# Kernel tuning notes

Measured on AMD Instinct MI355X. Metric: run time of the kernel, lower is better.

The kernel has to match this reference:

```python
import jax, jax.numpy as jnp
import numpy as np

N_HEADS = 16
D_MODEL = 1024
D_K = D_MODEL // N_HEADS
NEG_INF = -1e9


def setup_inputs() -> dict:
    key = jax.random.key(0)
    ks = jax.random.split(key, 7)
    B, S, D = 4, 2048, D_MODEL
    scale = 1.0 / np.sqrt(D)
    return {
        "query": jax.random.normal(ks[0], (B, S, D), dtype=jnp.float32),
        "key": jax.random.normal(ks[1], (B, S, D), dtype=jnp.float32),
        "value": jax.random.normal(ks[2], (B, S, D), dtype=jnp.float32),
        "Wq": jax.random.normal(ks[3], (D, D), dtype=jnp.float32) * scale,
        "Wk": jax.random.normal(ks[4], (D, D), dtype=jnp.float32) * scale,
        "Wv": jax.random.normal(ks[5], (D, D), dtype=jnp.float32) * scale,
        "Wo": jax.random.normal(ks[6], (D, D), dtype=jnp.float32) * scale,
    }


def _split_heads(x):
    # (B, S, D) -> (B, H, S, d_k)
    B, S, _ = x.shape
    return x.reshape(B, S, N_HEADS, D_K).transpose(0, 2, 1, 3)


def reference(query, key, value, Wq, Wk, Wv, Wo):
    B, S, D = query.shape
    # nn.Linear(d, d, bias=False): y = x @ W.T ; here W is stored as [out, in]
    Q = _split_heads(query @ Wq.T)
    K = _split_heads(key @ Wk.T)
    V = _split_heads(value @ Wv.T)
    scores = jnp.einsum("bhqd,bhkd->bhqk", Q, K) / jnp.sqrt(jnp.float32(D_K))
    # causal mask: 0 on/below diagonal, -1e9 above
    causal = jnp.where(
        jnp.tril(jnp.ones((S, S), dtype=bool)), 0.0, NEG_INF
    ).astype(scores.dtype)
    scores = scores + causal[None, None, :, :]
    attn = jax.nn.softmax(scores, axis=-1)
    heads = jnp.einsum("bhqk,bhkd->bhqd", attn, V)
    concat = heads.transpose(0, 2, 1, 3).reshape(B, S, D)
    out = concat @ Wo.T
    return out  # dropout p=0.0 -> identity
```

## Files before the change

kernel.cpp:

```cpp
#include <hip/hip_runtime.h>
#include <hip/hip_bf16.h>

typedef short short8 __attribute__((ext_vector_type(8)));
typedef short short4v __attribute__((ext_vector_type(4)));
typedef float floatx4 __attribute__((ext_vector_type(4)));

constexpr int BATCH = 4;
constexpr int SEQ = 2048;
constexpr int DMODEL = 1024;
constexpr int NHEADS = 16;
constexpr int DKH = 64;
constexpr int MROWS = BATCH * SEQ;
constexpr size_t NE = (size_t)MROWS * DMODEL;
constexpr size_t WE = (size_t)DMODEL * DMODEL;
constexpr float SC = 0.18033688011112042f;

__device__ __forceinline__ short f2bf(float f) {
    unsigned u = __float_as_uint(f);
    u += 0x7fffu + ((u >> 16) & 1u);
    return (short)(u >> 16);
}

__device__ __forceinline__ short2 pk2(float a, float b) {
    __hip_bfloat162 h = __float22bfloat162_rn(float2{a, b});
    short2 r;
    __builtin_memcpy(&r, &h, 4);
    return r;
}

__device__ __forceinline__ void ld16(const void* g, void* l) {
    __builtin_amdgcn_global_load_lds(
        (const __attribute__((address_space(1))) unsigned int*)g,
        (__attribute__((address_space(3))) unsigned int*)l, 16, 0, 0);
}

__global__ __launch_bounds__(256) void f32_to_bf16(const float* __restrict__ s,
                                                   short* __restrict__ d, int n4) {
    int i = blockIdx.x * blockDim.x + threadIdx.x;
    const int stride = gridDim.x * blockDim.x;
    for (; i < n4; i += stride) {
        float4 f = ((const float4*)s)[i];
        short4v v;
        v[0] = f2bf(f.x); v[1] = f2bf(f.y); v[2] = f2bf(f.z); v[3] = f2bf(f.w);
        ((short4v*)d)[i] = v;
    }
}

__global__ __launch_bounds__(256) void cvt2(const float* __restrict__ s0,
                                            const float* __restrict__ s1,
                                            short* __restrict__ d0,
                                            short* __restrict__ d1, int n4) {
    const float* s = blockIdx.y ? s1 : s0;
    short* d = blockIdx.y ? d1 : d0;
    int i = blockIdx.x * blockDim.x + threadIdx.x;
    const int stride = gridDim.x * blockDim.x;
    for (; i < n4; i += stride) {
        float4 f = ((const float4*)s)[i];
        short4v v;
        v[0] = f2bf(f.x); v[1] = f2bf(f.y); v[2] = f2bf(f.z); v[3] = f2bf(f.w);
        ((short4v*)d)[i] = v;
    }
}

__global__ __launch_bounds__(256) void wcvt3(const float* __restrict__ a,
                                             const float* __restrict__ b,
                                             const float* __restrict__ c,
                                             short* __restrict__ dst, int n4) {
    const float* s = (blockIdx.y == 0) ? a : (blockIdx.y == 1) ? b : c;
    short* d = dst + (size_t)blockIdx.y * (size_t)n4 * 4;
    int i = blockIdx.x * blockDim.x + threadIdx.x;
    const int stride = gridDim.x * blockDim.x;
    for (; i < n4; i += stride) {
        float4 f = ((const float4*)s)[i];
        short4v v;
        v[0] = f2bf(f.x); v[1] = f2bf(f.y); v[2] = f2bf(f.z); v[3] = f2bf(f.w);
        ((short4v*)d)[i] = v;
    }
}

template <int OUT_MODE, bool SCALEQ>
__global__ __launch_bounds__(256, 3) void gemm_nt(const short* __restrict__ A,
                                                  const short* __restrict__ B,
                                                  void* __restrict__ Yp) {
    __shared__ __align__(16) short Asw[128 * 32];
    __shared__ __align__(16) short Bsw[128 * 32];

    const int tid = threadIdx.x;
    const int w = tid >> 6, l = tid & 63;
    const int lane16 = l & 15, quad = l >> 4;
    const int wm = (w >> 1) * 64, wn = (w & 1) * 64;
    const int m0 = blockIdx.x * 128, n0 = blockIdx.y * 128;
    const int fsw = (lane16 >> 1) & 3;

    floatx4 acc[4][4];
#pragma unroll
    for (int i = 0; i < 4; ++i)
#pragma unroll
        for (int j = 0; j < 4; ++j) acc[i][j] = {0.f, 0.f, 0.f, 0.f};

    for (int k0 = 0; k0 < DMODEL; k0 += 32) {
#pragma unroll
        for (int i = 0; i < 2; ++i) {
            const int id = i * 256 + tid;
            const int row = id >> 2, ch = id & 3;
            const int sch = ch ^ ((row >> 1) & 3);
            ld16(A + (size_t)(m0 + row) * DMODEL + k0 + sch * 8,
                 Asw + (i * 256 + w * 64) * 8);
            ld16(B + (size_t)(n0 + row) * DMODEL + k0 + sch * 8,
                 Bsw + (i * 256 + w * 64) * 8);
        }
        __syncthreads();

        short8 af[4], bfr[4];
#pragma unroll
        for (int mi = 0; mi < 4; ++mi)
            af[mi] = *(const short8*)(Asw + (wm + mi * 16 + lane16) * 32 + (quad ^ fsw) * 8);
#pragma unroll
        for (int ni = 0; ni < 4; ++ni)
            bfr[ni] = *(const short8*)(Bsw + (wn + ni * 16 + lane16) * 32 + (quad ^ fsw) * 8);
#pragma unroll
        for (int mi = 0; mi < 4; ++mi)
#pragma unroll
            for (int ni = 0; ni < 4; ++ni)
                acc[mi][ni] = __builtin_amdgcn_mfma_f32_16x16x32_bf16(af[mi], bfr[ni],
                                                                      acc[mi][ni], 0, 0, 0);
        __syncthreads();
    }

    const int gmb = m0 + wm, gnb = n0 + wn;
    if (OUT_MODE == 0) {
        short* Y = (short*)Yp;
#pragma unroll
        for (int mi = 0; mi < 4; ++mi)
#pragma unroll
            for (int ni = 0; ni < 4; ++ni) {
                const int gm = gmb + mi * 16 + quad * 4;
                const int gn = gnb + ni * 16 + lane16;
#pragma unroll
                for (int r = 0; r < 4; ++r) {
                    const float val = SCALEQ ? acc[mi][ni][r] * SC : acc[mi][ni][r];
                    Y[(size_t)(gm + r) * DMODEL + gn] = f2bf(val);
                }
            }
    } else if (OUT_MODE == 1) {
        short* Y = (short*)Yp;
#pragma unroll
        for (int mi = 0; mi < 4; ++mi)
#pragma unroll
            for (int ni = 0; ni < 4; ++ni) {
                const int gm = gmb + mi * 16 + quad * 4;
                const int gn = gnb + ni * 16 + lane16;
                const int bb = gm >> 11, ss = gm & (SEQ - 1);
                const int hh = gn >> 6, dd = gn & 63;
                const size_t base = ((size_t)(bb * NHEADS + hh) * DKH + dd) * SEQ + ss;
                short4v vv;
#pragma unroll
                for (int r = 0; r < 4; ++r) vv[r] = f2bf(acc[mi][ni][r]);
                *(short4v*)(Y + base) = vv;
            }
    } else {
        float* Y = (float*)Yp;
#pragma unroll
        for (int mi = 0; mi < 4; ++mi)
#pragma unroll
            for (int ni = 0; ni < 4; ++ni) {
                const int gm = gmb + mi * 16 + quad * 4;
                const int gn = gnb + ni * 16 + lane16;
#pragma unroll
                for (int r = 0; r < 4; ++r)
                    Y[(size_t)(gm + r) * DMODEL + gn] = acc[mi][ni][r];
            }
    }
}

__global__ __launch_bounds__(256, 4) void attn_fwd(const short* __restrict__ Qb,
                                                   const short* __restrict__ Kb,
                                                   const short* __restrict__ Vt,
                                                   short* __restrict__ Oc) {
    __shared__ __align__(16) short Kl[2][64 * 64];
    __shared__ __align__(16) short Vl[2][64 * 64];
    __shared__ __align__(16) short Plds[4][16][64];

    const int bh = blockIdx.x;
    const int qt = (int)(gridDim.y - 1) - blockIdx.y;
    const int b = bh >> 4, h = bh & 15;
    const int tid = threadIdx.x;
    const int w = tid >> 6, l = tid & 63;
    const int lane16 = l & 15, quad = l >> 4;

    const short* Qrow =
        Qb + ((size_t)b * SEQ + qt * 64 + w * 16 + lane16) * DMODEL + h * DKH;
    const short8 qf0 = *(const short8*)(Qrow + quad * 8);
    const short8 qf1 = *(const short8*)(Qrow + 32 + quad * 8);

    const int r0 = tid >> 3, c0 = tid & 7;
    const int sc0 = c0 ^ (r0 & 7);
    const short* Kg = Kb + (size_t)b * SEQ * DMODEL + h * DKH;
    const short* Vg = Vt + (size_t)bh * DKH * SEQ;

    short8 kra, krb, vra, vrb;
    kra = *(const short8*)(Kg + (size_t)r0 * DMODEL + c0 * 8);
    krb = *(const short8*)(Kg + (size_t)(r0 + 32) * DMODEL + c0 * 8);
    vra = *(const short8*)(Vg + (size_t)r0 * SEQ + c0 * 8);
    vrb = *(const short8*)(Vg + (size_t)(r0 + 32) * SEQ + c0 * 8);
    *(short8*)&Kl[0][r0 * 64 + sc0 * 8] = kra;
    *(short8*)&Kl[0][(r0 + 32) * 64 + sc0 * 8] = krb;
    *(short8*)&Vl[0][r0 * 64 + sc0 * 8] = vra;
    *(short8*)&Vl[0][(r0 + 32) * 64 + sc0 * 8] = vrb;
    if (qt > 0) {
        kra = *(const short8*)(Kg + (size_t)(64 + r0) * DMODEL + c0 * 8);
        krb = *(const short8*)(Kg + (size_t)(64 + r0 + 32) * DMODEL + c0 * 8);
        vra = *(const short8*)(Vg + (size_t)r0 * SEQ + 64 + c0 * 8);
        vrb = *(const short8*)(Vg + (size_t)(r0 + 32) * SEQ + 64 + c0 * 8);
    }

    floatx4 oacc[4];
#pragma unroll
    for (int ni = 0; ni < 4; ++ni) oacc[ni] = {0.f, 0.f, 0.f, 0.f};
    float Lp = 0.f;
    const int swz = lane16 & 7;
    const int psw = lane16 & 7;

    for (int kt = 0; kt <= qt; ++kt) {
        const int cur = kt & 1;
        __syncthreads();
        if (kt < qt) {
            const int nb = cur ^ 1;
            *(short8*)&Kl[nb][r0 * 64 + sc0 * 8] = kra;
            *(short8*)&Kl[nb][(r0 + 32) * 64 + sc0 * 8] = krb;
            *(short8*)&Vl[nb][r0 * 64 + sc0 * 8] = vra;
            *(short8*)&Vl[nb][(r0 + 32) * 64 + sc0 * 8] = vrb;
            if (kt + 1 < qt) {
                const int kn = (kt + 2) * 64;
                kra = *(const short8*)(Kg + (size_t)(kn + r0) * DMODEL + c0 * 8);
                krb = *(const short8*)(Kg + (size_t)(kn + r0 + 32) * DMODEL + c0 * 8);
                vra = *(const short8*)(Vg + (size_t)r0 * SEQ + kn + c0 * 8);
                vrb = *(const short8*)(Vg + (size_t)(r0 + 32) * SEQ + kn + c0 * 8);
            }
        }

        float p[4][4];
#pragma unroll
        for (int nt = 0; nt < 4; ++nt) {
            const short* kr = &Kl[cur][(nt * 16 + lane16) * 64];
            floatx4 st = {0.f, 0.f, 0.f, 0.f};
            st = __builtin_amdgcn_mfma_f32_16x16x32_bf16(
                *(const short8*)(kr + (quad ^ swz) * 8), qf0, st, 0, 0, 0);
            st = __builtin_amdgcn_mfma_f32_16x16x32_bf16(
                *(const short8*)(kr + ((4 + quad) ^ swz) * 8), qf1, st, 0, 0, 0);
#pragma unroll
            for (int r = 0; r < 4; ++r) p[nt][r] = st[r];
        }

#pragma unroll
        for (int nt = 0; nt < 4; ++nt)
#pragma unroll
            for (int r = 0; r < 4; ++r) p[nt][r] = __builtin_amdgcn_exp2f(p[nt][r]);

        if (kt == qt) {
            const int qloc = w * 16 + lane16;
#pragma unroll
            for (int nt = 0; nt < 4; ++nt)
#pragma unroll
                for (int r = 0; r < 4; ++r)
                    if (nt * 16 + quad * 4 + r > qloc) p[nt][r] = 0.f;
        }

        float rs01 = 0.f, rs23 = 0.f;
#pragma unroll
        for (int nt = 0; nt < 4; ++nt)
#pragma unroll
            for (int r = 0; r < 4; ++r) {
                if (nt < 2) rs01 += p[nt][r]; else rs23 += p[nt][r];
            }
        Lp += rs01 + rs23;

#pragma unroll
        for (int nt = 0; nt < 4; ++nt) {
            const short2 lo = pk2(p[nt][0], p[nt][1]);
            const short2 hi = pk2(p[nt][2], p[nt][3]);
            short4v pk;
            pk[0] = lo.x; pk[1] = lo.y; pk[2] = hi.x; pk[3] = hi.y;
            const int pch = (nt * 2 + (quad >> 1)) ^ psw;
            *(short4v*)&Plds[w][lane16][pch * 8 + (quad & 1) * 4] = pk;
        }
        const short8 pf0 = *(const short8*)&Plds[w][lane16][(quad ^ psw) * 8];
        const short8 pf1 = *(const short8*)&Plds[w][lane16][((4 + quad) ^ psw) * 8];

#pragma unroll
        for (int ni = 0; ni < 4; ++ni) {
            const short* vr = &Vl[cur][(ni * 16 + lane16) * 64];
            oacc[ni] = __builtin_amdgcn_mfma_f32_16x16x32_bf16(
                pf0, *(const short8*)(vr + (quad ^ swz) * 8), oacc[ni], 0, 0, 0);
            oacc[ni] = __builtin_amdgcn_mfma_f32_16x16x32_bf16(
                pf1, *(const short8*)(vr + ((4 + quad) ^ swz) * 8), oacc[ni], 0, 0, 0);
        }
    }

    float L = Lp + __shfl_xor(Lp, 16);
    L += __shfl_xor(L, 32);
    float linv[4];
#pragma unroll
    for (int r = 0; r < 4; ++r) linv[r] = 1.f / __shfl(L, quad * 4 + r);
#pragma unroll
    for (int r = 0; r < 4; ++r) {
        const int qg = qt * 64 + w * 16 + quad * 4 + r;
#pragma unroll
        for (int ni = 0; ni < 4; ++ni)
            Oc[((size_t)b * SEQ + qg) * DMODEL + h * DKH + ni * 16 + lane16] =
                f2bf(oacc[ni][r] * linv[r]);
    }
}

extern "C" void kernel_launch(void* const* d_in, const int* in_sizes, int n_in,
                              void* d_out, int out_size, void* d_ws, size_t ws_size,
                              hipStream_t stream) {
    const float* q = (const float*)d_in[0];
    const float* k = (const float*)d_in[1];
    const float* v = (const float*)d_in[2];
    const float* Wq = (const float*)d_in[3];
    const float* Wk = (const float*)d_in[4];
    const float* Wv = (const float*)d_in[5];
    const float* Wo = (const float*)d_in[6];

    short* Qb = (short*)d_ws;
    short* Kb = Qb + NE;
    short* Vt = Kb + NE;
    short* Cc = Vt + NE;
    short* Wqb = (short*)d_out;
    short* Wkb = Wqb + WE;
    short* Wvb = Wqb + 2 * WE;
    short* Kbf = Wqb + 3 * WE;
    short* Wob = Vt;

    dim3 gg(MROWS / 128, DMODEL / 128);
    dim3 ga(BATCH * NHEADS, SEQ / 64);
    const int actN4 = (int)(NE / 4), wN4 = (int)(WE / 4);

    wcvt3<<<dim3(256, 3), 256, 0, stream>>>(Wq, Wk, Wv, (short*)d_out, wN4);
    cvt2<<<dim3(1024, 2), 256, 0, stream>>>(q, k, Cc, Kbf, actN4);
    gemm_nt<0, true><<<gg, 256, 0, stream>>>(Cc, Wqb, Qb);
    gemm_nt<0, false><<<gg, 256, 0, stream>>>(Kbf, Wkb, Kb);
    f32_to_bf16<<<2048, 256, 0, stream>>>(v, Cc, actN4);
    gemm_nt<1, false><<<gg, 256, 0, stream>>>(Cc, Wvb, Vt);
    attn_fwd<<<ga, 256, 0, stream>>>(Qb, Kb, Vt, Cc);
    f32_to_bf16<<<512, 256, 0, stream>>>(Wo, Wob, wN4);
    gemm_nt<2, false><<<gg, 256, 0, stream>>>(Cc, Wob, d_out);
}
```

Measured before the change: 313.4 us.

## Double-buffer GEMM LDS tiles, merge Q/K projections, fold Q scale into weights

Restructures the bf16 GEMM to prefetch the next K-tile into a second LDS buffer while computing on the current one, removing the load-then-sync stall each iteration. Q and K projections are launched as a single kernel over a z-dimension to reduce launch count and improve CU fill. The attention softmax scale is moved into the Wq conversion, dropping the multiply from the GEMM epilogue. LDS per block doubles, which may pressure occupancy, and scaling before bf16 rounding slightly changes numerics.

```diff
diff --git a/kernel.cpp b/kernel.cpp
--- a/kernel.cpp
+++ b/kernel.cpp
@@ -67,23 +67,25 @@
                                              const float* __restrict__ c,
                                              short* __restrict__ dst, int n4) {
     const float* s = (blockIdx.y == 0) ? a : (blockIdx.y == 1) ? b : c;
+    const float m = (blockIdx.y == 0) ? SC : 1.0f;
     short* d = dst + (size_t)blockIdx.y * (size_t)n4 * 4;
     int i = blockIdx.x * blockDim.x + threadIdx.x;
     const int stride = gridDim.x * blockDim.x;
     for (; i < n4; i += stride) {
         float4 f = ((const float4*)s)[i];
         short4v v;
-        v[0] = f2bf(f.x); v[1] = f2bf(f.y); v[2] = f2bf(f.z); v[3] = f2bf(f.w);
+        v[0] = f2bf(f.x * m); v[1] = f2bf(f.y * m);
+        v[2] = f2bf(f.z * m); v[3] = f2bf(f.w * m);
         ((short4v*)d)[i] = v;
     }
 }
 
-template <int OUT_MODE, bool SCALEQ>
-__global__ __launch_bounds__(256, 3) void gemm_nt(const short* __restrict__ A,
-                                                  const short* __restrict__ B,
-                                                  void* __restrict__ Yp) {
-    __shared__ __align__(16) short Asw[128 * 32];
-    __shared__ __align__(16) short Bsw[128 * 32];
+template <int OUT_MODE>
+__device__ __forceinline__ void gemm_body(const short* __restrict__ A,
+                                          const short* __restrict__ B,
+                                          void* __restrict__ Yp) {
+    __shared__ __align__(16) short Asw[2][128 * 32];
+    __shared__ __align__(16) short Bsw[2][128 * 32];
 
     const int tid = threadIdx.x;
     const int w = tid >> 6, l = tid & 63;
@@ -92,32 +94,42 @@
     const int m0 = blockIdx.x * 128, n0 = blockIdx.y * 128;
     const int fsw = (lane16 >> 1) & 3;
 
-    floatx4 acc[4][4];
-#pragma unroll
-    for (int i = 0; i < 4; ++i)
-#pragma unroll
-        for (int j = 0; j < 4; ++j) acc[i][j] = {0.f, 0.f, 0.f, 0.f};
-
-    for (int k0 = 0; k0 < DMODEL; k0 += 32) {
+    auto stage = [&](int k0, int bufi) {
 #pragma unroll
         for (int i = 0; i < 2; ++i) {
             const int id = i * 256 + tid;
             const int row = id >> 2, ch = id & 3;
             const int sch = ch ^ ((row >> 1) & 3);
             ld16(A + (size_t)(m0 + row) * DMODEL + k0 + sch * 8,
-                 Asw + (i * 256 + w * 64) * 8);
+                 &Asw[bufi][(i * 256 + w * 64) * 8]);
             ld16(B + (size_t)(n0 + row) * DMODEL + k0 + sch * 8,
-                 Bsw + (i * 256 + w * 64) * 8);
-        }
-        __syncthreads();
+                 &Bsw[bufi][(i * 256 + w * 64) * 8]);
+        }
+    };
+
+    floatx4 acc[4][4];
+#pragma unroll
+    for (int i = 0; i < 4; ++i)
+#pragma unroll
+        for (int j = 0; j < 4; ++j) acc[i][j] = {0.f, 0.f, 0.f, 0.f};
+
+    constexpr int NT = DMODEL / 32;
+    stage(0, 0);
+    __syncthreads();
+
+    for (int t = 0; t < NT; ++t) {
+        const int cur = t & 1;
+        if (t + 1 < NT) stage((t + 1) * 32, cur ^ 1);
 
         short8 af[4], bfr[4];
 #pragma unroll
         for (int mi = 0; mi < 4; ++mi)
-            af[mi] = *(const short8*)(Asw + (wm + mi * 16 + lane16) * 32 + (quad ^ fsw) * 8);
+            af[mi] = *(const short8*)(&Asw[cur][(wm + mi * 16 + lane16) * 32 +
+                                                ((quad ^ fsw) * 8)]);
 #pragma unroll
         for (int ni = 0; ni < 4; ++ni)
-            bfr[ni] = *(const short8*)(Bsw + (wn + ni * 16 + lane16) * 32 + (quad ^ fsw) * 8);
+            bfr[ni] = *(const short8*)(&Bsw[cur][(wn + ni * 16 + lane16) * 32 +
+                                                 ((quad ^ fsw) * 8)]);
 #pragma unroll
         for (int mi = 0; mi < 4; ++mi)
 #pragma unroll
@@ -137,10 +149,8 @@
                 const int gm = gmb + mi * 16 + quad * 4;
                 const int gn = gnb + ni * 16 + lane16;
 #pragma unroll
-                for (int r = 0; r < 4; ++r) {
-                    const float val = SCALEQ ? acc[mi][ni][r] * SC : acc[mi][ni][r];
-                    Y[(size_t)(gm + r) * DMODEL + gn] = f2bf(val);
-                }
+                for (int r = 0; r < 4; ++r)
+                    Y[(size_t)(gm + r) * DMODEL + gn] = f2bf(acc[mi][ni][r]);
             }
     } else if (OUT_MODE == 1) {
         short* Y = (short*)Yp;
@@ -171,6 +181,22 @@
                     Y[(size_t)(gm + r) * DMODEL + gn] = acc[mi][ni][r];
             }
     }
+}
+
+template <int OUT_MODE>
+__global__ __launch_bounds__(256, 3) void gemm_nt(const short* __restrict__ A,
+                                                  const short* __restrict__ B,
+                                                  void* __restrict__ Yp) {
+    gemm_body<OUT_MODE>(A, B, Yp);
+}
+
+__global__ __launch_bounds__(256, 3) void gemm_qk(const short* __restrict__ Aq,
+                                                  const short* __restrict__ Ak,
+                                                  const short* __restrict__ Wqk,
+                                                  short* __restrict__ Yq,
+                                                  short* __restrict__ Yk) {
+    const int z = blockIdx.z;
+    gemm_body<0>(z ? Ak : Aq, Wqk + (size_t)z * WE, z ? Yk : Yq);
 }
 
 __global__ __launch_bounds__(256, 4) void attn_fwd(const short* __restrict__ Qb,
@@ -334,16 +360,16 @@
     short* Wob = Vt;
 
     dim3 gg(MROWS / 128, DMODEL / 128);
+    dim3 gqk(MROWS / 128, DMODEL / 128, 2);
     dim3 ga(BATCH * NHEADS, SEQ / 64);
     const int actN4 = (int)(NE / 4), wN4 = (int)(WE / 4);
 
     wcvt3<<<dim3(256, 3), 256, 0, stream>>>(Wq, Wk, Wv, (short*)d_out, wN4);
     cvt2<<<dim3(1024, 2), 256, 0, stream>>>(q, k, Cc, Kbf, actN4);
-    gemm_nt<0, true><<<gg, 256, 0, stream>>>(Cc, Wqb, Qb);
-    gemm_nt<0, false><<<gg, 256, 0, stream>>>(Kbf, Wkb, Kb);
+    gemm_qk<<<gqk, 256, 0, stream>>>(Cc, Kbf, Wqb, Qb, Kb);
     f32_to_bf16<<<2048, 256, 0, stream>>>(v, Cc, actN4);
-    gemm_nt<1, false><<<gg, 256, 0, stream>>>(Cc, Wvb, Vt);
+    gemm_nt<1><<<gg, 256, 0, stream>>>(Cc, Wvb, Vt);
     attn_fwd<<<ga, 256, 0, stream>>>(Qb, Kb, Vt, Cc);
     f32_to_bf16<<<512, 256, 0, stream>>>(Wo, Wob, wN4);
-    gemm_nt<2, false><<<gg, 256, 0, stream>>>(Cc, Wob, d_out);
-}
+    gemm_nt<2><<<gg, 256, 0, stream>>>(Cc, Wob, d_out);
+}
```

New measurement: 312.0 us. No clear change (-0.4%).
